# Optimization experiments

Measured on AMD Instinct MI355X. Metric: run time of the kernel, lower is better.

## Reference

```python
import jax, jax.numpy as jnp
import numpy as np


def setup_inputs() -> dict:
    key = jax.random.key(0)
    k1, k2 = jax.random.split(key)
    B, C, H, W, K = 8, 32, 224, 224, 5
    x = jax.random.normal(k1, (B, C, H, W), dtype=jnp.float32)
    kernel = jax.random.normal(k2, (C, 1, K, K), dtype=jnp.float32) * 0.1
    return {"x": x, "kernel": kernel, "stride": 1, "padding": 2, "dilation": 1}


def reference(x, kernel, stride, padding, dilation):
    # Tropical-max (morphological dilation) conv: out[p] = max_k (x[p+k] + w_flipped[k]).
    # is_max=True, softmax_temp=None -> hard max; kernel is flipped (true convolution).
    B, C, H, W = x.shape
    OC, _, K, _ = kernel.shape
    neutral = -jnp.inf
    x_pad = jnp.pad(x, ((0, 0), (0, 0), (padding, padding), (padding, padding)),
                    constant_values=neutral)
    Hp, Wp = H + 2 * padding, W + 2 * padding
    H_out = (Hp - dilation * (K - 1) - 1) // stride + 1
    W_out = (Wp - dilation * (K - 1) - 1) // stride + 1
    wflip = kernel[:, 0, ::-1, ::-1]  # (C, K, K) flipped, as in torch kernel.flip((2,3))
    # Start from neutral: matches the extra neutral row padded onto the unfold tensor.
    out = jnp.full((B, C, H_out, W_out), neutral, dtype=x.dtype)
    for i in range(K):  # small fixed K*K loop; avoids materializing the (B,C,K^2,HW) unfold
        for j in range(K):
            patch = x_pad[:, :,
                          i * dilation: i * dilation + (H_out - 1) * stride + 1: stride,
                          j * dilation: j * dilation + (W_out - 1) * stride + 1: stride]
            out = jnp.maximum(out, patch + wflip[:, i, j][None, :, None, None])
    return out
```

## Files before the change

### kernel.cpp

```cpp
#include <hip/hip_runtime.h>
#include <math.h>


#define TC_B 8
#define TC_C 32
#define TC_H 224
#define TC_W 224
#define TC_WQ 56
#define TC_HG 14
#define T_ROWS 20
#define ROW_F4 65
#define ROW_FL (ROW_F4 * 4)

__global__ __launch_bounds__(256) void tropical_conv2d_kernel(
    const float* __restrict__ x, const float* __restrict__ kern,
    float* __restrict__ out) {
  const int tid = threadIdx.x;
  const int lane = tid & 63;
  const int yl = tid >> 6;
  const int blk = blockIdx.x;
  const int hg = blk % TC_HG;
  const int bc = blk / TC_HG;
  const int c = bc & (TC_C - 1);

  __shared__ float tile[T_ROWS * ROW_FL];

  const float NEG = -INFINITY;
  const float4 NINF4 = make_float4(NEG, NEG, NEG, NEG);
  const float* xp = x + (size_t)bc * (TC_H * TC_W);

  if (tid < T_ROWS) *(float4*)&tile[tid * ROW_FL] = NINF4;

  const int cl = lane < TC_WQ ? lane : TC_WQ - 1;
  #pragma unroll
  for (int rr = 0; rr < 5; ++rr) {
    const int r = yl * 5 + rr;
    const int g = hg * 16 - 2 + r;
    float* ldsrow = &tile[r * ROW_FL + 4];
    if (g >= 0 && g < TC_H) {
      const float* gp = xp + (size_t)g * TC_W + cl * 4;
      __builtin_amdgcn_global_load_lds(
          (const __attribute__((address_space(1))) void*)gp,
          (__attribute__((address_space(3))) void*)ldsrow, 16, 0, 0);
    } else {
      *(float4*)(ldsrow + (size_t)lane * 4) = NINF4;
    }
  }

  float w[25];
  #pragma unroll
  for (int q = 0; q < 25; ++q) w[q] = kern[c * 25 + 24 - q];

  __syncthreads();

  if (lane >= TC_WQ) return;

  const int hbase = hg * 16 + yl * 4;

  float acc[4][4];
  #pragma unroll
  for (int o = 0; o < 4; ++o)
    #pragma unroll
    for (int k = 0; k < 4; ++k) acc[o][k] = NEG;

  const bool redge = (lane == TC_WQ - 1);

  #pragma unroll
  for (int ri = 0; ri < 8; ++ri) {
    const float* rp = &tile[(yl * 4 + ri) * ROW_FL + 4 * lane];
    const float4 A = *(const float4*)(rp);
    const float4 Bv = *(const float4*)(rp + 4);
    const float4 Cv = *(const float4*)(rp + 8);
    float v[12] = {A.x, A.y, A.z, A.w, Bv.x, Bv.y, Bv.z, Bv.w,
                   Cv.x, Cv.y, Cv.z, Cv.w};
    v[8] = redge ? NEG : v[8];
    v[9] = redge ? NEG : v[9];

    #pragma unroll
    for (int o = 0; o < 4; ++o) {
      const int i = ri - o;
      if (i < 0 || i > 4) continue;
      #pragma unroll
      for (int k = 0; k < 4; ++k) {
        const float t0 = v[2 + k] + w[i * 5 + 0];
        const float t1 = v[3 + k] + w[i * 5 + 1];
        const float t2 = v[4 + k] + w[i * 5 + 2];
        const float t3 = v[5 + k] + w[i * 5 + 3];
        const float t4 = v[6 + k] + w[i * 5 + 4];
        acc[o][k] = fmaxf(fmaxf(fmaxf(acc[o][k], t0), t1),
                          fmaxf(fmaxf(t2, t3), t4));
      }
    }
  }

  float* op = out + (size_t)bc * (TC_H * TC_W) + (size_t)hbase * TC_W;
  #pragma unroll
  for (int o = 0; o < 4; ++o) {
    ((float4*)(op + (size_t)o * TC_W))[lane] =
        make_float4(acc[o][0], acc[o][1], acc[o][2], acc[o][3]);
  }
}

extern "C" void kernel_launch(void* const* d_in, const int* in_sizes, int n_in,
                              void* d_out, int out_size, void* d_ws, size_t ws_size,
                              hipStream_t stream) {
  const float* x = (const float*)d_in[0];
  const float* k = (const float*)d_in[1];
  float* out = (float*)d_out;

  dim3 block(256, 1, 1);
  dim3 grid(TC_B * TC_C * TC_HG, 1, 1);
  tropical_conv2d_kernel<<<grid, block, 0, stream>>>(x, k, out);
}
```

Before: 110.3 us.

## Replace LDS tile staging with direct global loads per thread

Removes the shared-memory tile, the async global-to-LDS loads and the block barrier. Each thread now reads its own input rows straight from global memory as one float4 plus two float2 halo loads, and handles the boundary rows and columns with branches. The max tree is also reshaped to expose more independent ops. This drops the synchronization and LDS traffic but relies on L1/L2 caching for the overlapping rows and halos, which now cost redundant global loads.

Measured after the change: 115.7 us. 1.05x slower.

```diff
diff --git a/kernel.cpp b/kernel.cpp
--- a/kernel.cpp
+++ b/kernel.cpp
@@ -8,9 +8,6 @@
 #define TC_W 224
 #define TC_WQ 56
 #define TC_HG 14
-#define T_ROWS 20
-#define ROW_F4 65
-#define ROW_FL (ROW_F4 * 4)
 
 __global__ __launch_bounds__(256) void tropical_conv2d_kernel(
     const float* __restrict__ x, const float* __restrict__ kern,
@@ -23,38 +20,15 @@
   const int bc = blk / TC_HG;
   const int c = bc & (TC_C - 1);
 
-  __shared__ float tile[T_ROWS * ROW_FL];
-
   const float NEG = -INFINITY;
-  const float4 NINF4 = make_float4(NEG, NEG, NEG, NEG);
-  const float* xp = x + (size_t)bc * (TC_H * TC_W);
-
-  if (tid < T_ROWS) *(float4*)&tile[tid * ROW_FL] = NINF4;
-
-  const int cl = lane < TC_WQ ? lane : TC_WQ - 1;
-  #pragma unroll
-  for (int rr = 0; rr < 5; ++rr) {
-    const int r = yl * 5 + rr;
-    const int g = hg * 16 - 2 + r;
-    float* ldsrow = &tile[r * ROW_FL + 4];
-    if (g >= 0 && g < TC_H) {
-      const float* gp = xp + (size_t)g * TC_W + cl * 4;
-      __builtin_amdgcn_global_load_lds(
-          (const __attribute__((address_space(1))) void*)gp,
-          (__attribute__((address_space(3))) void*)ldsrow, 16, 0, 0);
-    } else {
-      *(float4*)(ldsrow + (size_t)lane * 4) = NINF4;
-    }
-  }
 
   float w[25];
   #pragma unroll
   for (int q = 0; q < 25; ++q) w[q] = kern[c * 25 + 24 - q];
 
-  __syncthreads();
-
   if (lane >= TC_WQ) return;
 
+  const float* xp = x + (size_t)bc * (TC_H * TC_W);
   const int hbase = hg * 16 + yl * 4;
 
   float acc[4][4];
@@ -63,18 +37,24 @@
     #pragma unroll
     for (int k = 0; k < 4; ++k) acc[o][k] = NEG;
 
+  const bool ledge = (lane == 0);
   const bool redge = (lane == TC_WQ - 1);
+  const int col0 = lane * 4;
 
   #pragma unroll
   for (int ri = 0; ri < 8; ++ri) {
-    const float* rp = &tile[(yl * 4 + ri) * ROW_FL + 4 * lane];
-    const float4 A = *(const float4*)(rp);
-    const float4 Bv = *(const float4*)(rp + 4);
-    const float4 Cv = *(const float4*)(rp + 8);
-    float v[12] = {A.x, A.y, A.z, A.w, Bv.x, Bv.y, Bv.z, Bv.w,
-                   Cv.x, Cv.y, Cv.z, Cv.w};
-    v[8] = redge ? NEG : v[8];
-    v[9] = redge ? NEG : v[9];
+    const int g = hbase - 2 + ri;
+    if (g < 0 || g >= TC_H) continue;
+    const float* rowp = xp + (size_t)g * TC_W;
+
+    const float4 Bv = *(const float4*)(rowp + col0);
+    float2 A2, C2;
+    if (ledge) { A2 = make_float2(NEG, NEG); }
+    else       { A2 = *(const float2*)(rowp + col0 - 2); }
+    if (redge) { C2 = make_float2(NEG, NEG); }
+    else       { C2 = *(const float2*)(rowp + col0 + 4); }
+
+    const float u[8] = {A2.x, A2.y, Bv.x, Bv.y, Bv.z, Bv.w, C2.x, C2.y};
 
     #pragma unroll
     for (int o = 0; o < 4; ++o) {
@@ -82,13 +62,12 @@
       if (i < 0 || i > 4) continue;
       #pragma unroll
       for (int k = 0; k < 4; ++k) {
-        const float t0 = v[2 + k] + w[i * 5 + 0];
-        const float t1 = v[3 + k] + w[i * 5 + 1];
-        const float t2 = v[4 + k] + w[i * 5 + 2];
-        const float t3 = v[5 + k] + w[i * 5 + 3];
-        const float t4 = v[6 + k] + w[i * 5 + 4];
-        acc[o][k] = fmaxf(fmaxf(fmaxf(acc[o][k], t0), t1),
-                          fmaxf(fmaxf(t2, t3), t4));
+        const float m01 = fmaxf(u[k + 0] + w[i * 5 + 0],
+                                u[k + 1] + w[i * 5 + 1]);
+        const float m23 = fmaxf(u[k + 2] + w[i * 5 + 2],
+                                u[k + 3] + w[i * 5 + 3]);
+        const float m4  = u[k + 4] + w[i * 5 + 4];
+        acc[o][k] = fmaxf(fmaxf(acc[o][k], m01), fmaxf(m23, m4));
       }
     }
   }
```
